# Performance work log

Measured on AMD Instinct MI355X. Metric: run time of the kernel, lower is better.

Reference implementation:

```python
import jax, jax.numpy as jnp
import numpy as np

H = 4096      # num_patches (sequence length)
WS = 8        # window_size
SHIFT = 4     # shift_size
NH = 8        # num_heads
DIM = 512     # embedding dim
HD = DIM // NH
NW = H // WS  # windows per batch element
B = 16
LN_EPS = 1e-5


def _layer_norm(x, g, b):
    m = jnp.mean(x, axis=-1, keepdims=True)
    v = jnp.var(x, axis=-1, keepdims=True)
    return (x - m) * jax.lax.rsqrt(v + LN_EPS) * g + b


def _window_partition(x):
    # Faithful to the repo: reshape->permute(nW<->ws)->flatten, giving strided windows.
    Bx, N, C = x.shape
    return x.reshape(Bx, N // WS, WS, C).transpose(0, 2, 1, 3).reshape(-1, WS, C)


def _window_reverse(w, N, Bx):
    C = w.shape[-1]
    return w.reshape(Bx, N // WS, WS, C).transpose(0, 2, 1, 3).reshape(Bx, N, C)


def _attn_mask():
    # Built exactly as in __init__ (numpy, constant at trace time): (NW, WS, WS)
    m = np.zeros((1, H, 1), np.float32)
    m[:, :H - WS] = 0.0
    m[:, H - WS:H - SHIFT] = 1.0
    m[:, H - SHIFT:] = 2.0
    mw = m.reshape(1, NW, WS, 1).transpose(0, 2, 1, 3).reshape(-1, WS)  # (NW, WS)
    d = mw[:, None, :] - mw[:, :, None]
    return np.where(d != 0, np.float32(-100.0), np.float32(0.0))


def _forward(x, norm1_g, norm1_b, qkv_w, qkv_b, proj_w, proj_b,
             norm2_g, norm2_b, fc1_w, fc1_b, fc2_w, fc2_b):
    Bx = x.shape[0]
    shortcut = x
    xn = _layer_norm(x, norm1_g, norm1_b)
    xs = jnp.roll(xn, -SHIFT, axis=1)
    xw = _window_partition(xs)                       # (Bx*NW, WS, DIM)
    B_ = xw.shape[0]
    qkv = xw @ qkv_w.T + qkv_b                       # (B_, WS, 3*DIM)
    qkv = qkv.reshape(B_, WS, 3, NH, HD).transpose(2, 0, 3, 1, 4)
    q, k, v = qkv[0], qkv[1], qkv[2]                 # (B_, NH, WS, HD)
    attn = jnp.einsum('bhqd,bhkd->bhqk', q, k) * (HD ** -0.5)
    mask = jnp.asarray(_attn_mask())                 # (NW, WS, WS)
    attn = attn.reshape(B_ // NW, NW, NH, WS, WS) + mask[None, :, None]
    attn = jax.nn.softmax(attn.reshape(B_, NH, WS, WS), axis=-1)
    o = jnp.einsum('bhqk,bhkd->bqhd', attn, v).reshape(B_, WS, DIM)
    o = o @ proj_w.T + proj_b
    xr = _window_reverse(o, H, Bx)
    xr = jnp.roll(xr, SHIFT, axis=1)
    x1 = shortcut + xr
    h = _layer_norm(x1, norm2_g, norm2_b)
    h = jax.nn.gelu(h @ fc1_w.T + fc1_b, approximate=False)
    h = h @ fc2_w.T + fc2_b
    return x1 + h


def setup_inputs() -> dict:
    key = jax.random.key(0)
    ks = jax.random.split(key, 8)
    s = 0.02
    return {
        'x': jax.random.normal(ks[0], (B, H, DIM), jnp.float32),
        'norm1_g': jnp.ones((DIM,), jnp.float32),
        'norm1_b': jnp.zeros((DIM,), jnp.float32),
        'qkv_w': jax.random.normal(ks[1], (3 * DIM, DIM), jnp.float32) * s,
        'qkv_b': jnp.zeros((3 * DIM,), jnp.float32),
        'proj_w': jax.random.normal(ks[2], (DIM, DIM), jnp.float32) * s,
        'proj_b': jnp.zeros((DIM,), jnp.float32),
        'norm2_g': jnp.ones((DIM,), jnp.float32),
        'norm2_b': jnp.zeros((DIM,), jnp.float32),
        'fc1_w': jax.random.normal(ks[3], (4 * DIM, DIM), jnp.float32) * s,
        'fc1_b': jnp.zeros((4 * DIM,), jnp.float32),
        'fc2_w': jax.random.normal(ks[4], (DIM, 4 * DIM), jnp.float32) * s,
        'fc2_b': jnp.zeros((DIM,), jnp.float32),
    }


def reference(x, norm1_g, norm1_b, qkv_w, qkv_b, proj_w, proj_b,
              norm2_g, norm2_b, fc1_w, fc1_b, fc2_w, fc2_b):
    return _forward(x, norm1_g, norm1_b, qkv_w, qkv_b, proj_w, proj_b,
                    norm2_g, norm2_b, fc1_w, fc1_b, fc2_w, fc2_b)
```

## Files before the change

### kernel.cpp

```cpp
#include <hip/hip_runtime.h>
#include <hip/hip_bf16.h>
#include <math.h>

typedef unsigned short ushortT;
typedef __attribute__((ext_vector_type(8))) short short8;
typedef __attribute__((ext_vector_type(4))) short short4v;
typedef __attribute__((ext_vector_type(4))) float f32x4;
typedef __attribute__((ext_vector_type(4))) float float4v;

#define TOK 65536
#define NSEQ 4096
#define DIM 512

__device__ __forceinline__ float bf2f(ushortT u) {
  union { float f; unsigned int i; } v; v.i = ((unsigned int)u) << 16; return v.f;
}
__device__ __forceinline__ ushortT f2bf(float f) {
  union { float f; unsigned int i; } v; v.f = f;
  unsigned int r = v.i + 0x7fffu + ((v.i >> 16) & 1u);
  return (ushortT)(r >> 16);
}

__device__ __forceinline__ float fast_gelu(float x) {
  const float y = fabsf(x) * 0.70710678118654752f;
  const float t = __builtin_amdgcn_rcpf(__builtin_fmaf(0.3275911f, y, 1.f));
  float p = 1.061405429f;
  p = __builtin_fmaf(p, t, -1.453152027f);
  p = __builtin_fmaf(p, t, 1.421413741f);
  p = __builtin_fmaf(p, t, -0.284496736f);
  p = __builtin_fmaf(p, t, 0.254829592f);
  p = p * t;
  const float e = __builtin_amdgcn_exp2f(-y * y * 1.4426950408889634f);
  float erfv = __builtin_fmaf(-p, e, 1.f);
  erfv = copysignf(erfv, x);
  return 0.5f * x * (1.f + erfv);
}

#define GLOAD_LDS(gp, lp) __builtin_amdgcn_global_load_lds( \
    (const __attribute__((address_space(1))) unsigned int*)(gp), \
    (__attribute__((address_space(3))) unsigned int*)(lp), 16, 0, 0)

#define LGKM0 do { asm volatile("s_waitcnt lgkmcnt(0)" ::: "memory"); \
                   __builtin_amdgcn_sched_barrier(0); } while (0)
#define BAR __builtin_amdgcn_s_barrier()
#define VMC(n) asm volatile("s_waitcnt vmcnt(" #n ")" ::: "memory")
#define SB0 __builtin_amdgcn_sched_barrier(0)

__global__ void cvt_kernel(const float* __restrict__ in, ushortT* __restrict__ out, int n4) {
  int i = blockIdx.x * 256 + threadIdx.x;
  if (i >= n4) return;
  float4v v = *(const float4v*)(in + (size_t)i * 4);
  short4v o;
#pragma unroll
  for (int j = 0; j < 4; ++j) o[j] = (short)f2bf(v[j]);
  *(short4v*)(out + (size_t)i * 4) = o;
}

template <bool INBF>
__global__ __launch_bounds__(256)
void ln_kernel(const void* __restrict__ inp, const float* __restrict__ gw,
               const float* __restrict__ bw, ushortT* __restrict__ out)
{
  const int lane = threadIdx.x & 63;
  const size_t tok = (size_t)blockIdx.x * 4 + (threadIdx.x >> 6);
  const int col = lane * 8;
  float x[8];
  if constexpr (INBF) {
    short8 v = *(const short8*)((const ushortT*)inp + tok * DIM + col);
#pragma unroll
    for (int j = 0; j < 8; ++j) x[j] = bf2f((ushortT)v[j]);
  } else {
    const float* p = (const float*)inp + tok * DIM + col;
    float4v a = *(const float4v*)p, b = *(const float4v*)(p + 4);
#pragma unroll
    for (int j = 0; j < 4; ++j) { x[j] = a[j]; x[4 + j] = b[j]; }
  }
  float s = 0.f, ss = 0.f;
#pragma unroll
  for (int j = 0; j < 8; ++j) { s += x[j]; ss += x[j] * x[j]; }
#pragma unroll
  for (int off = 1; off < 64; off <<= 1) {
    s += __shfl_xor(s, off, 64);
    ss += __shfl_xor(ss, off, 64);
  }
  const float mean = s * (1.f / 512.f);
  const float var = ss * (1.f / 512.f) - mean * mean;
  const float rstd = rsqrtf(var + 1e-5f);
  float4v g1 = *(const float4v*)(gw + col), g2 = *(const float4v*)(gw + col + 4);
  float4v b1 = *(const float4v*)(bw + col), b2 = *(const float4v*)(bw + col + 4);
  short8 o;
#pragma unroll
  for (int j = 0; j < 4; ++j) {
    o[j]     = (short)f2bf((x[j]     - mean) * rstd * g1[j] + b1[j]);
    o[4 + j] = (short)f2bf((x[4 + j] - mean) * rstd * g2[j] + b2[j]);
  }
  *(short8*)(out + tok * DIM + col) = o;
}

#define MFMA_PHASE(MH) \
  _Pragma("unroll") \
  for (int m_ = 0; m_ < 4; ++m_) \
    _Pragma("unroll") \
    for (int n_ = 0; n_ < 4; ++n_) \
      acc[(MH) * 4 + m_][n_] = __builtin_amdgcn_mfma_f32_16x16x32_bf16( \
          Af[m_], Bf[n_], acc[(MH) * 4 + m_][n_], 0, 0, 0)

#define STAGE_A2(bufp, h, gptr) do { \
    GLOAD_LDS((gptr) + (size_t)((h) * 128) * K,     (bufp) + (h) * 8192 + w * 1024); \
    GLOAD_LDS((gptr) + (size_t)((h) * 128 + 8) * K, (bufp) + (h) * 8192 + w * 1024 + 512); \
  } while (0)
#define STAGE_B2(bufp, h, gptr) do { \
    GLOAD_LDS((gptr) + (size_t)((h) * 128) * K,     (bufp) + (h) * 8192 + w * 1024); \
    GLOAD_LDS((gptr) + (size_t)((h) * 128 + 8) * K, (bufp) + (h) * 8192 + w * 1024 + 512); \
  } while (0)

template <int EPI>
__global__ __launch_bounds__(512, 2)
void gemm256(const ushortT* __restrict__ A, const ushortT* __restrict__ Bt,
             const float* __restrict__ bias, int M, int N, int K,
             ushortT* __restrict__ outb, float* __restrict__ outf,
             const float* __restrict__ resf, const ushortT* __restrict__ resb)
{
  __shared__ __align__(16) ushortT sm[65536];
  ushortT* const Ab0 = sm;
  ushortT* const Ab1 = sm + 16384;
  ushortT* const Bb0 = sm + 32768;
  ushortT* const Bb1 = sm + 49152;

  const int tid = threadIdx.x;
  const int w = tid >> 6, l = tid & 63;
  const int wr = w >> 2, wc = w & 3;

  const int nwg = gridDim.x * gridDim.y;
  int wg = blockIdx.y * gridDim.x + blockIdx.x;
  {
    const int q = nwg >> 3, r8 = nwg & 7;
    const int xc = wg & 7, yc = wg >> 3;
    wg = (xc < r8 ? xc * (q + 1) : r8 * (q + 1) + (xc - r8) * q) + yc;
  }
  const int nbn = N >> 8;
  const int mb = wg / nbn, nb = wg % nbn;
  const int m0 = mb << 8, n0 = nb << 8;
  const int NT = K >> 6;

  const ushortT* gA = A  + (size_t)(m0 + w * 16 + (l >> 3)) * K + (((l & 7) ^ (l >> 3)) << 3);
  const ushortT* gB = Bt + (size_t)(n0 + w * 16 + (l >> 3)) * K + (((l & 7) ^ (l >> 3)) << 3);

  const int rl = l & 15, ql = l >> 4;
  const int aoff = (wr * 128 + rl) * 64;
  const int boff = (wc * 64 + rl) * 64;
  const int cs0 = ((ql) ^ (l & 7)) << 3;
  const int cs1 = ((4 + ql) ^ (l & 7)) << 3;

  f32x4 acc[8][4];
  const f32x4 zero = {0.f, 0.f, 0.f, 0.f};
#pragma unroll
  for (int i = 0; i < 8; ++i)
#pragma unroll
    for (int j = 0; j < 4; ++j) acc[i][j] = zero;

  ushortT* Ac = Ab0; ushortT* An = Ab1;
  ushortT* Bc = Bb0; ushortT* Bn = Bb1;

  STAGE_A2(Ac, 0, gA); STAGE_A2(Ac, 1, gA);
  STAGE_B2(Bc, 0, gB); STAGE_B2(Bc, 1, gB);
  VMC(0);
  BAR;

  short8 Af[4], Bf[4];
  size_t koff = 64;

  for (int t = 0; t < NT; ++t) {
#pragma unroll
    for (int m = 0; m < 4; ++m) Af[m] = *(const short8*)(Ac + aoff + m * 1024 + cs0);
#pragma unroll
    for (int n = 0; n < 4; ++n) Bf[n] = *(const short8*)(Bc + boff + n * 1024 + cs0);
    if (t + 1 < NT) {
      STAGE_A2(An, 0, gA + koff); STAGE_A2(An, 1, gA + koff);
      STAGE_B2(Bn, 0, gB + koff); STAGE_B2(Bn, 1, gB + koff);
    }
    SB0; BAR; LGKM0;
    __builtin_amdgcn_s_setprio(1);
    MFMA_PHASE(0);
    __builtin_amdgcn_s_setprio(0);
#pragma unroll
    for (int m = 0; m < 4; ++m) Af[m] = *(const short8*)(Ac + aoff + (4 + m) * 1024 + cs0);
    SB0; BAR; LGKM0;
    __builtin_amdgcn_s_setprio(1);
    MFMA_PHASE(1);
    __builtin_amdgcn_s_setprio(0);
#pragma unroll
    for (int m = 0; m < 4; ++m) Af[m] = *(const short8*)(Ac + aoff + m * 1024 + cs1);
#pragma unroll
    for (int n = 0; n < 4; ++n) Bf[n] = *(const short8*)(Bc + boff + n * 1024 + cs1);
    SB0; BAR; LGKM0;
    __builtin_amdgcn_s_setprio(1);
    MFMA_PHASE(0);
    __builtin_amdgcn_s_setprio(0);
#pragma unroll
    for (int m = 0; m < 4; ++m) Af[m] = *(const short8*)(Ac + aoff + (4 + m) * 1024 + cs1);
    SB0; BAR; LGKM0;
    __builtin_amdgcn_s_setprio(1);
    MFMA_PHASE(1);
    __builtin_amdgcn_s_setprio(0);
    if (t + 1 < NT) VMC(0);
    BAR;
    ushortT* tp;
    tp = Ac; Ac = An; An = tp;
    tp = Bc; Bc = Bn; Bn = tp;
    koff += 64;
  }

  float* const ep = (float*)sm;
#pragma unroll
  for (int p = 0; p < 2; ++p) {
    if (p) BAR;
    if (wr == p) {
#pragma unroll
      for (int m = 0; m < 8; ++m) {
#pragma unroll
        for (int n = 0; n < 4; ++n) {
          const int c = wc * 64 + n * 16 + rl;
          const int pc = c ^ (c >> 3);
          *(f32x4*)(ep + (m * 4 + ql) * 1024 + pc * 4) = acc[m][n];
        }
      }
    }
    BAR;
#pragma unroll
    for (int k = 0; k < 4; ++k) {
      const int rb = w + k * 8;
      const int rowb = 16 * (rb >> 2) + 4 * (rb & 3);
      f32x4 rv[4];
#pragma unroll
      for (int j = 0; j < 4; ++j) {
        const int c = 4 * l + j;
        const int pc = c ^ (c >> 3);
        rv[j] = *(const f32x4*)(ep + rb * 1024 + pc * 4);
      }
      const int col = n0 + 4 * l;
      const float4v bb = *(const float4v*)(bias + col);
#pragma unroll
      for (int i = 0; i < 4; ++i) {
        const size_t row = (size_t)(m0 + p * 128 + rowb + i);
        float v0 = rv[0][i] + bb[0], v1 = rv[1][i] + bb[1],
              v2 = rv[2][i] + bb[2], v3 = rv[3][i] + bb[3];
        if constexpr (EPI == 1) {
          const float4v rr = *(const float4v*)(resf + row * (size_t)N + col);
          v0 += rr[0]; v1 += rr[1]; v2 += rr[2]; v3 += rr[3];
        }
        if constexpr (EPI == 2) {
          v0 = fast_gelu(v0); v1 = fast_gelu(v1); v2 = fast_gelu(v2); v3 = fast_gelu(v3);
        }
        if constexpr (EPI == 3) {
          const short4v rb4 = *(const short4v*)(resb + row * (size_t)N + col);
          v0 += bf2f((ushortT)rb4[0]); v1 += bf2f((ushortT)rb4[1]);
          v2 += bf2f((ushortT)rb4[2]); v3 += bf2f((ushortT)rb4[3]);
          float4v o = {v0, v1, v2, v3};
          *(float4v*)(outf + row * (size_t)N + col) = o;
        } else {
          short4v o;
          o[0] = (short)f2bf(v0); o[1] = (short)f2bf(v1);
          o[2] = (short)f2bf(v2); o[3] = (short)f2bf(v3);
          *(short4v*)(outb + row * (size_t)N + col) = o;
        }
      }
    }
  }
}

__global__ __launch_bounds__(512)
void attn_kernel(const ushortT* __restrict__ qkv, ushortT* __restrict__ out)
{
  __shared__ __align__(16) ushortT sq[8][1544];
  const int wb = blockIdx.x;
  const int b  = wb >> 9;
  const int rr = wb & 511;
  const int w1 = rr >> 6;
  const int g  = rr & 63;
  const int tid = threadIdx.x;

#pragma unroll
  for (int c = 0; c < 3; ++c) {
    const int f = c * 512 + tid;
    const int i = f / 192;
    const int col = (f % 192) * 8;
    const int tin = (64 * g + 8 * i + w1 + 4) & (NSEQ - 1);
    const ushortT* src = qkv + ((size_t)b * NSEQ + tin) * 1536 + col;
    *(short8*)(&sq[i][col]) = *(const short8*)src;
  }
  __syncthreads();

  const int wave = tid >> 6, lane = tid & 63;
  const int h = wave;
  const int qi = lane >> 3, kj = lane & 7;

  float s = 0.f;
  const ushortT* qrow = &sq[qi][h * 64];
  const ushortT* krow = &sq[kj][512 + h * 64];
#pragma unroll
  for (int c = 0; c < 8; ++c) {
    short8 qa = *(const short8*)(qrow + c * 8);
    short8 ka = *(const short8*)(krow + c * 8);
#pragma unroll
    for (int j = 0; j < 8; ++j) s += bf2f((ushortT)qa[j]) * bf2f((ushortT)ka[j]);
  }
  s *= 0.125f;

  const int pq = 64 * g + 8 * qi + w1;
  const int pk = 64 * g + 8 * kj + w1;
  const int cq = (pq < 4088) ? 0 : (pq < 4092 ? 1 : 2);
  const int ck = (pk < 4088) ? 0 : (pk < 4092 ? 1 : 2);
  if (cq != ck) s -= 100.f;

  float mx = s;
  mx = fmaxf(mx, __shfl_xor(mx, 1, 64));
  mx = fmaxf(mx, __shfl_xor(mx, 2, 64));
  mx = fmaxf(mx, __shfl_xor(mx, 4, 64));
  const float e = expf(s - mx);
  float sum = e;
  sum += __shfl_xor(sum, 1, 64);
  sum += __shfl_xor(sum, 2, 64);
  sum += __shfl_xor(sum, 4, 64);
  const float p = e / sum;

  const int dc = lane & 7;
  float o[8];
#pragma unroll
  for (int j = 0; j < 8; ++j) o[j] = 0.f;
#pragma unroll
  for (int k2 = 0; k2 < 8; ++k2) {
    const float pk2 = __shfl(p, (lane & ~7) + k2, 64);
    short8 va = *(const short8*)(&sq[k2][1024 + h * 64 + dc * 8]);
#pragma unroll
    for (int j = 0; j < 8; ++j) o[j] += pk2 * bf2f((ushortT)va[j]);
  }

  const int tout = (512 * qi + 64 * w1 + g + 4) & (NSEQ - 1);
  short8 ov;
#pragma unroll
  for (int j = 0; j < 8; ++j) ov[j] = (short)f2bf(o[j]);
  *(short8*)(out + ((size_t)b * NSEQ + tout) * DIM + h * 64 + dc * 8) = ov;
}

extern "C" void kernel_launch(void* const* d_in, const int* in_sizes, int n_in,
                              void* d_out, int out_size, void* d_ws, size_t ws_size,
                              hipStream_t stream) {
  const float* x      = (const float*)d_in[0];
  const float* n1g    = (const float*)d_in[1];
  const float* n1b    = (const float*)d_in[2];
  const float* qkv_w  = (const float*)d_in[3];
  const float* qkv_b  = (const float*)d_in[4];
  const float* proj_w = (const float*)d_in[5];
  const float* proj_b = (const float*)d_in[6];
  const float* n2g    = (const float*)d_in[7];
  const float* n2b    = (const float*)d_in[8];
  const float* fc1_w  = (const float*)d_in[9];
  const float* fc1_b  = (const float*)d_in[10];
  const float* fc2_w  = (const float*)d_in[11];
  const float* fc2_b  = (const float*)d_in[12];
  float* out = (float*)d_out;

  size_t off = 0;
  char* ws = (char*)d_ws;
  auto alloc = [&](size_t b) { void* p = ws + off; off += (b + 255) & ~(size_t)255; return p; };

  ushortT* qkvw_b = (ushortT*)alloc((size_t)1536 * 512 * 2);
  ushortT* projw_b = (ushortT*)alloc((size_t)512 * 512 * 2);
  ushortT* fc1w_b = (ushortT*)alloc((size_t)2048 * 512 * 2);
  ushortT* fc2w_b = (ushortT*)alloc((size_t)512 * 2048 * 2);
  ushortT* bufA = (ushortT*)alloc((size_t)TOK * 512 * 2);
  ushortT* bufQ = (ushortT*)alloc((size_t)TOK * 1536 * 2);
  ushortT* x1 = bufQ;

  int nch = 1;
  while (nch < 16) {
    size_t need = (size_t)(TOK / nch) * 2048 * 2;
    if (off + need <= ws_size) break;
    nch <<= 1;
  }
  ushortT* h1 = (ushortT*)(ws + off);

  cvt_kernel<<<(1536 * 512 / 4 + 255) / 256, 256, 0, stream>>>(qkv_w, qkvw_b, 1536 * 512 / 4);
  cvt_kernel<<<(512 * 512 / 4 + 255) / 256, 256, 0, stream>>>(proj_w, projw_b, 512 * 512 / 4);
  cvt_kernel<<<(2048 * 512 / 4 + 255) / 256, 256, 0, stream>>>(fc1_w, fc1w_b, 2048 * 512 / 4);
  cvt_kernel<<<(512 * 2048 / 4 + 255) / 256, 256, 0, stream>>>(fc2_w, fc2w_b, 512 * 2048 / 4);

  ln_kernel<false><<<TOK / 4, 256, 0, stream>>>(x, n1g, n1b, bufA);

  gemm256<0><<<dim3(TOK / 256, 1536 / 256), 512, 0, stream>>>(
      bufA, qkvw_b, qkv_b, TOK, 1536, 512, bufQ, nullptr, nullptr, nullptr);

  attn_kernel<<<8192, 512, 0, stream>>>(bufQ, bufA);

  gemm256<1><<<dim3(TOK / 256, 512 / 256), 512, 0, stream>>>(
      bufA, projw_b, proj_b, TOK, 512, 512, x1, nullptr, x, nullptr);

  ln_kernel<true><<<TOK / 4, 256, 0, stream>>>(x1, n2g, n2b, bufA);

  const int tc = TOK / nch;
  for (int c = 0; c < nch; ++c) {
    const ushortT* hin = bufA + (size_t)c * tc * 512;
    gemm256<2><<<dim3(tc / 256, 2048 / 256), 512, 0, stream>>>(
        hin, fc1w_b, fc1_b, tc, 2048, 512, h1, nullptr, nullptr, nullptr);
    gemm256<3><<<dim3(tc / 256, 512 / 256), 512, 0, stream>>>(
        h1, fc2w_b, fc2_b, tc, 512, 2048, nullptr, out + (size_t)c * tc * 512,
        nullptr, x1 + (size_t)c * tc * 512);
  }
}
```

Baseline: 695.1 us.

## Software-pipeline LDS fragment reads in GEMM loop with partial lgkmcnt waits

The GEMM main loop now issues LDS fragment reads as inline-asm ds_read_b128 with immediate offsets from precomputed byte addresses. It drops the three intra-iteration barriers and full lgkmcnt(0) waits in favour of partial lgkmcnt waits. The reads for the next MFMA quad are issued while the current quad runs, and the first fragments of the next K-tile are prefetched right after the buffer-swap barrier. This aims to hide LDS latency behind MFMA work and cut barrier stalls. In exchange it relies on hand-counted waitcnt values and an assumed LDS base address of zero, which is fragile if other memory operations or the compiler reorder LDS traffic.

```diff
diff --git a/kernel.cpp b/kernel.cpp
--- a/kernel.cpp
+++ b/kernel.cpp
@@ -40,11 +40,14 @@
     (const __attribute__((address_space(1))) unsigned int*)(gp), \
     (__attribute__((address_space(3))) unsigned int*)(lp), 16, 0, 0)
 
-#define LGKM0 do { asm volatile("s_waitcnt lgkmcnt(0)" ::: "memory"); \
-                   __builtin_amdgcn_sched_barrier(0); } while (0)
 #define BAR __builtin_amdgcn_s_barrier()
 #define VMC(n) asm volatile("s_waitcnt vmcnt(" #n ")" ::: "memory")
 #define SB0 __builtin_amdgcn_sched_barrier(0)
+#define STR2(x) #x
+#define DSR(dst, addr, IMM) \
+  asm volatile("ds_read_b128 %0, %1 offset:" STR2(IMM) : "=v"(dst) : "v"(addr))
+#define LGKM(n) do { asm volatile("s_waitcnt lgkmcnt(" #n ")" ::: "memory"); \
+                     __builtin_amdgcn_sched_barrier(0); } while (0)
 
 __global__ void cvt_kernel(const float* __restrict__ in, ushortT* __restrict__ out, int n4) {
   int i = blockIdx.x * 256 + threadIdx.x;
@@ -97,14 +100,6 @@
   *(short8*)(out + tok * DIM + col) = o;
 }
 
-#define MFMA_PHASE(MH) \
-  _Pragma("unroll") \
-  for (int m_ = 0; m_ < 4; ++m_) \
-    _Pragma("unroll") \
-    for (int n_ = 0; n_ < 4; ++n_) \
-      acc[(MH) * 4 + m_][n_] = __builtin_amdgcn_mfma_f32_16x16x32_bf16( \
-          Af[m_], Bf[n_], acc[(MH) * 4 + m_][n_], 0, 0, 0)
-
 #define STAGE_A2(bufp, h, gptr) do { \
     GLOAD_LDS((gptr) + (size_t)((h) * 128) * K,     (bufp) + (h) * 8192 + w * 1024); \
     GLOAD_LDS((gptr) + (size_t)((h) * 128 + 8) * K, (bufp) + (h) * 8192 + w * 1024 + 512); \
@@ -113,6 +108,23 @@
     GLOAD_LDS((gptr) + (size_t)((h) * 128) * K,     (bufp) + (h) * 8192 + w * 1024); \
     GLOAD_LDS((gptr) + (size_t)((h) * 128 + 8) * K, (bufp) + (h) * 8192 + w * 1024 + 512); \
   } while (0)
+
+#define DSR_KS0() do { \
+    DSR(AfX[0], adrA, 0);    DSR(AfX[1], adrA, 2048); \
+    DSR(AfX[2], adrA, 4096); DSR(AfX[3], adrA, 6144); \
+    DSR(BfC[0], adrB, 0);    DSR(BfC[1], adrB, 2048); \
+    DSR(BfC[2], adrB, 4096); DSR(BfC[3], adrB, 6144); \
+    DSR(AfY[0], adrA, 8192);  DSR(AfY[1], adrA, 10240); \
+    DSR(AfY[2], adrA, 12288); DSR(AfY[3], adrA, 14336); \
+  } while (0)
+
+#define QUAD(AF, BF, MB) \
+  _Pragma("unroll") \
+  for (int m_ = 0; m_ < 4; ++m_) \
+    _Pragma("unroll") \
+    for (int n_ = 0; n_ < 4; ++n_) \
+      acc[(MB) + m_][n_] = __builtin_amdgcn_mfma_f32_16x16x32_bf16( \
+          AF[m_], BF[n_], acc[(MB) + m_][n_], 0, 0, 0)
 
 template <int EPI>
 __global__ __launch_bounds__(512, 2)
@@ -147,10 +159,11 @@
   const ushortT* gB = Bt + (size_t)(n0 + w * 16 + (l >> 3)) * K + (((l & 7) ^ (l >> 3)) << 3);
 
   const int rl = l & 15, ql = l >> 4;
-  const int aoff = (wr * 128 + rl) * 64;
-  const int boff = (wc * 64 + rl) * 64;
-  const int cs0 = ((ql) ^ (l & 7)) << 3;
-  const int cs1 = ((4 + ql) ^ (l & 7)) << 3;
+  const int cchunk = (ql ^ (l & 7)) << 4;
+  unsigned adrA  = (unsigned)((wr * 128 + rl) * 128 + cchunk);
+  unsigned adrB  = (unsigned)(65536 + (wc * 64 + rl) * 128 + cchunk);
+  unsigned adrA1 = adrA ^ 64;
+  unsigned adrB1 = adrB ^ 64;
 
   f32x4 acc[8][4];
   const f32x4 zero = {0.f, 0.f, 0.f, 0.f};
@@ -167,48 +180,47 @@
   VMC(0);
   BAR;
 
-  short8 Af[4], Bf[4];
+  short8 AfX[4], AfY[4], BfC[4];
+  short8 AfX2[4], AfY2[4], BfN[4];
   size_t koff = 64;
 
+  DSR_KS0();
+
   for (int t = 0; t < NT; ++t) {
-#pragma unroll
-    for (int m = 0; m < 4; ++m) Af[m] = *(const short8*)(Ac + aoff + m * 1024 + cs0);
-#pragma unroll
-    for (int n = 0; n < 4; ++n) Bf[n] = *(const short8*)(Bc + boff + n * 1024 + cs0);
     if (t + 1 < NT) {
       STAGE_A2(An, 0, gA + koff); STAGE_A2(An, 1, gA + koff);
       STAGE_B2(Bn, 0, gB + koff); STAGE_B2(Bn, 1, gB + koff);
     }
-    SB0; BAR; LGKM0;
+    LGKM(4);
     __builtin_amdgcn_s_setprio(1);
-    MFMA_PHASE(0);
+    QUAD(AfX, BfC, 0);
     __builtin_amdgcn_s_setprio(0);
-#pragma unroll
-    for (int m = 0; m < 4; ++m) Af[m] = *(const short8*)(Ac + aoff + (4 + m) * 1024 + cs0);
-    SB0; BAR; LGKM0;
+    DSR(AfX2[0], adrA1, 0);    DSR(AfX2[1], adrA1, 2048);
+    DSR(AfX2[2], adrA1, 4096); DSR(AfX2[3], adrA1, 6144);
+    DSR(BfN[0], adrB1, 0);     DSR(BfN[1], adrB1, 2048);
+    DSR(BfN[2], adrB1, 4096);  DSR(BfN[3], adrB1, 6144);
+    LGKM(8);
     __builtin_amdgcn_s_setprio(1);
-    MFMA_PHASE(1);
+    QUAD(AfY, BfC, 4);
     __builtin_amdgcn_s_setprio(0);
-#pragma unroll
-    for (int m = 0; m < 4; ++m) Af[m] = *(const short8*)(Ac + aoff + m * 1024 + cs1);
-#pragma unroll
-    for (int n = 0; n < 4; ++n) Bf[n] = *(const short8*)(Bc + boff + n * 1024 + cs1);
-    SB0; BAR; LGKM0;
+    DSR(AfY2[0], adrA1, 8192);  DSR(AfY2[1], adrA1, 10240);
+    DSR(AfY2[2], adrA1, 12288); DSR(AfY2[3], adrA1, 14336);
+    LGKM(4);
     __builtin_amdgcn_s_setprio(1);
-    MFMA_PHASE(0);
+    QUAD(AfX2, BfN, 0);
     __builtin_amdgcn_s_setprio(0);
-#pragma unroll
-    for (int m = 0; m < 4; ++m) Af[m] = *(const short8*)(Ac + aoff + (4 + m) * 1024 + cs1);
-    SB0; BAR; LGKM0;
+    LGKM(0);
     __builtin_amdgcn_s_setprio(1);
-    MFMA_PHASE(1);
+    QUAD(AfY2, BfN, 4);
     __builtin_amdgcn_s_setprio(0);
     if (t + 1 < NT) VMC(0);
     BAR;
     ushortT* tp;
     tp = Ac; Ac = An; An = tp;
     tp = Bc; Bc = Bn; Bn = tp;
+    adrA ^= 0x8000; adrB ^= 0x8000; adrA1 ^= 0x8000; adrB1 ^= 0x8000;
     koff += 64;
+    if (t + 1 < NT) DSR_KS0();
   }
 
   float* const ep = (float*)sm;
```

New measurement: 682.1 us. No clear change (-1.9%).
